# Kernel optimization log

Measured on AMD Instinct MI355X. Metric: run time of the kernel, lower is better.

The kernel has to match this reference:

```python
import jax, jax.numpy as jnp
import numpy as np

COMMITMENT_COST = 0.25
ENTROPY_LOSS_WEIGHT = 0.1
EPSILON = 1e-05
NUM_EMBEDDINGS = 2048
EMBEDDING_DIM = 64


def setup_inputs() -> dict:
    key = jax.random.key(0)
    kx, ke = jax.random.split(key)
    x = jax.random.normal(kx, (16, 64, 64, EMBEDDING_DIM), dtype=jnp.float32)
    embedding = jax.random.normal(ke, (NUM_EMBEDDINGS, EMBEDDING_DIM), dtype=jnp.float32)
    return {"x": x, "embedding": embedding}


def reference(x, embedding):
    input_shape = x.shape
    flat_x = x.reshape(-1, EMBEDDING_DIM)              # [N, D]
    distances = (jnp.sum(flat_x ** 2, axis=1, keepdims=True)
                 + jnp.sum(embedding ** 2, axis=1)
                 - 2.0 * jnp.matmul(flat_x, embedding.T))
    encoding_indices = jnp.argmin(distances, axis=1)   # [N]
    quantized = embedding[encoding_indices].reshape(input_shape)

    commitment_loss = jnp.mean((jax.lax.stop_gradient(quantized) - x) ** 2)
    codebook_loss = jnp.mean((quantized - jax.lax.stop_gradient(x)) ** 2)
    # straight-through estimator
    quantized = x + jax.lax.stop_gradient(quantized - x)

    # histogram of code usage == mean of one-hot encodings (scatter-add, avoids [N,K] one-hot)
    n_tokens = flat_x.shape[0]
    counts = jnp.zeros((NUM_EMBEDDINGS,), dtype=flat_x.dtype).at[encoding_indices].add(1.0)
    avg_probs = counts / n_tokens
    perplexity = jnp.exp(-jnp.sum(avg_probs * jnp.log(avg_probs + EPSILON)))
    entropy_loss = jnp.sum(avg_probs * jnp.log(avg_probs + EPSILON))

    vq_loss = codebook_loss + COMMITMENT_COST * commitment_loss + ENTROPY_LOSS_WEIGHT * entropy_loss
    return (quantized, vq_loss, commitment_loss, codebook_loss, perplexity,
            entropy_loss, encoding_indices.reshape(input_shape[:-1]), avg_probs)
```

## Files before the change

kernel.cpp:

```cpp
#include <hip/hip_runtime.h>
#include <float.h>

typedef _Float16 half8 __attribute__((ext_vector_type(8)));
typedef float    f32x4 __attribute__((ext_vector_type(4)));

constexpr int N_TOK = 65536;
constexpr int D     = 64;
constexpr int K     = 2048;
constexpr int TILE_C = 64;
constexpr int NTILE  = K / TILE_C;
constexpr int TOK_PER_BLK = 64;
constexpr int NBLK = N_TOK / TOK_PER_BLK;
constexpr float EPS_RESCORE = 0.15f;

constexpr size_t QN       = (size_t)N_TOK * D;
constexpr size_t SCAL_OFF = QN;
constexpr size_t IDX_OFF  = QN + 5;
constexpr size_t PROB_OFF = IDX_OFF + N_TOK;

constexpr size_t WS_HNORM = 0;
constexpr size_t WS_COUNT = 8192;
constexpr size_t WS_BSUM  = 16384;
constexpr size_t WS_SW    = 24576;
constexpr int REC_B  = 40;
constexpr int TILE_B = 256 * REC_B;

__device__ inline unsigned long long pack_key(float d, int k) {
    unsigned u = __float_as_uint(d);
    u = (u & 0x80000000u) ? ~u : (u | 0x80000000u);
    return ((unsigned long long)u << 32) | (unsigned)k;
}

__device__ inline float unpack_dist(unsigned long long key) {
    unsigned u = (unsigned)(key >> 32);
    u = (u & 0x80000000u) ? (u & 0x7FFFFFFFu) : ~u;
    return __uint_as_float(u);
}

__device__ inline unsigned long long shfl_xor_u64_w16(unsigned long long v, int m) {
    int lo = __shfl_xor((int)(unsigned)v, m, 16);
    int hi = __shfl_xor((int)(unsigned)(v >> 32), m, 16);
    return ((unsigned long long)(unsigned)hi << 32) | (unsigned)lo;
}

__global__ __launch_bounds__(256) void vq_init(const float* __restrict__ emb,
                                               float* __restrict__ hnorm,
                                               unsigned* __restrict__ counts,
                                               double* __restrict__ blocksums,
                                               char* __restrict__ swb) {
    const int g  = blockIdx.x * 256 + threadIdx.x;
    const int r  = g >> 3;
    const int c0 = g & 7;
    const float4* p4 = (const float4*)(emb + (size_t)r * D + 8 * c0);
    float4 q0 = p4[0], q1 = p4[1];
    float v[8] = {q0.x, q0.y, q0.z, q0.w, q1.x, q1.y, q1.z, q1.w};
    half8 h;
    float s = 0.f;
#pragma unroll
    for (int i = 0; i < 8; ++i) {
        s += v[i] * v[i];
        h[i] = (_Float16)v[i];
    }
    const int t    = r >> 6;
    const int w    = (r >> 4) & 3;
    const int m16  = r & 15;
    const int lane = (c0 & 3) * 16 + m16;
    const int slot = c0 >> 2;
    char* rec = swb + (size_t)(t * 256 + w * 64 + lane) * REC_B;
    *(half8*)(rec + slot * 16) = h;

#pragma unroll
    for (int off = 1; off < 8; off <<= 1) s += __shfl_xor(s, off, 8);
    if (c0 < 4) *(float*)(rec + 32) = 0.5f * s;
    if (c0 == 0) hnorm[r] = 0.5f * s;
    if (g < K) counts[g] = 0u;
    if (g < NBLK) blocksums[g] = 0.0;
}

#define ISSUE(P0, P1, HN)                                                          \
  {                                                                                \
    asm volatile("global_load_dwordx4 %0, %3, off\n\t"                             \
                 "global_load_dwordx4 %1, %3, off offset:16\n\t"                   \
                 "global_load_dword   %2, %3, off offset:32"                       \
                 : "=&v"(P0), "=&v"(P1), "=&v"(HN)                                 \
                 : "v"(pl));                                                       \
    pl += TILE_B;                                                                  \
  }

#define WAITC(N)                                                                   \
  asm volatile("s_waitcnt vmcnt(" #N ")" ::: "memory");                            \
  __builtin_amdgcn_sched_barrier(0);

#define VQ_STEP(P0, P1, HN, TT)                                                    \
  {                                                                                \
    f32x4 acc[4];                                                                  \
    __builtin_amdgcn_s_setprio(1);                                                 \
    _Pragma("unroll")                                                              \
    for (int a = 0; a < 4; ++a) {                                                  \
      acc[a] = (f32x4){(HN), (HN), (HN), (HN)};                                    \
      acc[a] = __builtin_amdgcn_mfma_f32_16x16x32_f16(axh[a][0], P0, acc[a], 0, 0, 0); \
      acc[a] = __builtin_amdgcn_mfma_f32_16x16x32_f16(axh[a][1], P1, acc[a], 0, 0, 0); \
    }                                                                              \
    __builtin_amdgcn_s_setprio(0);                                                 \
    _Pragma("unroll")                                                              \
    for (int a = 0; a < 4; ++a)                                                    \
      _Pragma("unroll")                                                            \
      for (int r = 0; r < 4; ++r) {                                                \
        unsigned _kb = (__float_as_uint(acc[a][r]) & 0xFFFFFFE0u) | (unsigned)(TT);\
        float _f = __uint_as_float(_kb);                                           \
        best2[a][r] = fminf(best2[a][r], fmaxf(best1[a][r], _f));                  \
        best1[a][r] = fminf(best1[a][r], _f);                                      \
      }                                                                            \
  }

__global__ __launch_bounds__(256, 2) void vq_fused(const float* __restrict__ x,
                                                   const float* __restrict__ emb,
                                                   const float* __restrict__ hnorm,
                                                   const char* __restrict__ swb,
                                                   unsigned* __restrict__ counts,
                                                   double* __restrict__ blocksums,
                                                   float* __restrict__ out) {
    __shared__ unsigned long long kls[64][10];
    __shared__ int bks[64];
    __shared__ double wsum[4];

    const int tid  = threadIdx.x;
    const int lane = tid & 63;
    const int wav  = tid >> 6;
    const int t0   = blockIdx.x * TOK_PER_BLK;
    const int m16  = lane & 15;
    const int g    = lane >> 4;
    const int ko   = g * 8;
    const int cit  = wav * 16 + m16;

    half8 axh[4][2];
#pragma unroll
    for (int a = 0; a < 4; ++a) {
        const float* xr = x + (size_t)(t0 + 16 * a + m16) * D;
#pragma unroll
        for (int c = 0; c < 2; ++c) {
            const float4* p4 = (const float4*)(xr + 32 * c + ko);
            float4 q0 = p4[0], q1 = p4[1];
            float v[8] = {q0.x, q0.y, q0.z, q0.w, q1.x, q1.y, q1.z, q1.w};
            half8 h;
#pragma unroll
            for (int j = 0; j < 8; ++j) h[j] = (_Float16)(-v[j]);
            axh[a][c] = h;
        }
    }

    float best1[4][4], best2[4][4];
#pragma unroll
    for (int a = 0; a < 4; ++a)
#pragma unroll
        for (int r = 0; r < 4; ++r) { best1[a][r] = FLT_MAX; best2[a][r] = FLT_MAX; }

    const char* pl = swb + (size_t)tid * REC_B;

    half8 A0, A1;  float hA;
    half8 B0, B1;  float hB;
    half8 C0, C1;  float hC;

    ISSUE(A0, A1, hA);
    ISSUE(B0, B1, hB);

    for (int t = 0; t < 28; t += 3) {
        ISSUE(C0, C1, hC);
        WAITC(6);
        VQ_STEP(A0, A1, hA, t);
        ISSUE(A0, A1, hA);
        WAITC(6);
        VQ_STEP(B0, B1, hB, t + 1);
        ISSUE(B0, B1, hB);
        WAITC(6);
        VQ_STEP(C0, C1, hC, t + 2);
    }
    WAITC(3);
    VQ_STEP(A0, A1, hA, 30);
    WAITC(0);
    VQ_STEP(B0, B1, hB, 31);

#pragma unroll
    for (int a = 0; a < 4; ++a)
#pragma unroll
        for (int r = 0; r < 4; ++r) {
            const unsigned b1 = __float_as_uint(best1[a][r]);
            const unsigned b2 = __float_as_uint(best2[a][r]);
            unsigned long long k1 = pack_key(best1[a][r], (int)(b1 & 31u) * TILE_C + cit);
            unsigned long long k2 = pack_key(best2[a][r], (int)(b2 & 31u) * TILE_C + cit);
#pragma unroll
            for (int off = 8; off; off >>= 1) {
                unsigned long long o1 = shfl_xor_u64_w16(k1, off);
                unsigned long long o2 = shfl_xor_u64_w16(k2, off);
                unsigned long long hi1 = (k1 > o1) ? k1 : o1;
                unsigned long long lo2 = (k2 < o2) ? k2 : o2;
                k1 = (k1 < o1) ? k1 : o1;
                k2 = (hi1 < lo2) ? hi1 : lo2;
            }
            if (m16 == 0) {
                kls[16 * a + g * 4 + r][wav]     = k1;
                kls[16 * a + g * 4 + r][4 + wav] = k2;
            }
        }
    __syncthreads();

    if (tid < 64) {
        float ds[8]; int kk[8];
        unsigned long long kmin = ~0ULL;
#pragma unroll
        for (int w = 0; w < 8; ++w) {
            unsigned long long key = kls[tid][w];
            ds[w] = unpack_dist(key);
            kk[w] = (int)(unsigned)(key & 0xFFFFFFFFu);
            if (key < kmin) kmin = key;
        }
        int bk = (int)(unsigned)(kmin & 0xFFFFFFFFu);
        const float fmin = unpack_dist(kmin);
        int cnt = 0;
#pragma unroll
        for (int w = 0; w < 8; ++w) cnt += (ds[w] <= fmin + EPS_RESCORE) ? 1 : 0;

        if (cnt > 1) {
            unsigned long long bkey = ~0ULL;
            const float* xr = x + (size_t)(t0 + tid) * D;
            for (int w = 0; w < 8; ++w) {
                if (ds[w] <= fmin + EPS_RESCORE) {
                    const int k = kk[w];
                    const float* cr = emb + (size_t)k * D;
                    float s0 = 0.f, s1 = 0.f, s2 = 0.f, s3 = 0.f;
#pragma unroll
                    for (int i = 0; i < 16; ++i) {
                        s0 = fmaf(cr[4 * i + 0], xr[4 * i + 0], s0);
                        s1 = fmaf(cr[4 * i + 1], xr[4 * i + 1], s1);
                        s2 = fmaf(cr[4 * i + 2], xr[4 * i + 2], s2);
                        s3 = fmaf(cr[4 * i + 3], xr[4 * i + 3], s3);
                    }
                    float hd = hnorm[k] - ((s0 + s1) + (s2 + s3));
                    unsigned long long key = pack_key(hd, k);
                    if (key < bkey) bkey = key;
                }
            }
            bk = (int)(unsigned)(bkey & 0xFFFFFFFFu);
        }
        bks[tid] = bk;
        out[IDX_OFF + t0 + tid] = (float)bk;
        atomicAdd(&counts[bk], 1u);
    }
    __syncthreads();

    const int tok = tid >> 2;
    const int i4  = tid & 3;
    const int bk  = bks[tok];
    const float4* xr4 = (const float4*)(x + (size_t)(t0 + tok) * D);
    const float4* cr4 = (const float4*)(emb + (size_t)bk * D);
    float4* qr4 = (float4*)(out + (size_t)(t0 + tok) * D);
    float local = 0.f;
#pragma unroll
    for (int ii = 0; ii < 4; ++ii) {
        const int idx = i4 + 4 * ii;
        float4 xv = xr4[idx];
        float4 cv = cr4[idx];
        float dx = cv.x - xv.x, dy = cv.y - xv.y;
        float dz = cv.z - xv.z, dw = cv.w - xv.w;
        local += dx * dx + dy * dy + dz * dz + dw * dw;
        float4 q;
        q.x = xv.x + dx; q.y = xv.y + dy;
        q.z = xv.z + dz; q.w = xv.w + dw;
        qr4[idx] = q;
    }
    double ld = (double)local;
#pragma unroll
    for (int off = 32; off > 0; off >>= 1) ld += __shfl_down(ld, off, 64);
    if (lane == 0) wsum[wav] = ld;
    __syncthreads();
    if (tid == 0)
        blocksums[blockIdx.x] = (wsum[0] + wsum[1]) + (wsum[2] + wsum[3]);
}

__global__ __launch_bounds__(256) void vq_finalize(const unsigned* __restrict__ counts,
                                                   const double* __restrict__ blocksums,
                                                   float* __restrict__ out) {
    const int tid = threadIdx.x;
    double e = 0.0;
#pragma unroll
    for (int i = 0; i < 8; ++i) {
        int k = tid + i * 256;
        float p = (float)counts[k] / 65536.0f;
        out[PROB_OFF + k] = p;
        double pd = (double)p;
        e += pd * log(pd + 1e-5);
    }
    double s = 0.0;
#pragma unroll
    for (int i = 0; i < NBLK / 256; ++i) s += blocksums[tid + i * 256];
#pragma unroll
    for (int off = 32; off > 0; off >>= 1) {
        e += __shfl_down(e, off, 64);
        s += __shfl_down(s, off, 64);
    }
    __shared__ double we[4], ws2[4];
    int lane = tid & 63, wid = tid >> 6;
    if (lane == 0) { we[wid] = e; ws2[wid] = s; }
    __syncthreads();
    if (tid == 0) {
        double entropy = (we[0] + we[1]) + (we[2] + we[3]);
        double sumsq   = (ws2[0] + ws2[1]) + (ws2[2] + ws2[3]);
        double mse     = sumsq / (double)((size_t)N_TOK * D);
        out[SCAL_OFF + 0] = (float)(1.25 * mse + 0.1 * entropy);
        out[SCAL_OFF + 1] = (float)mse;
        out[SCAL_OFF + 2] = (float)mse;
        out[SCAL_OFF + 3] = (float)exp(-entropy);
        out[SCAL_OFF + 4] = (float)entropy;
    }
}

extern "C" void kernel_launch(void* const* d_in, const int* in_sizes, int n_in,
                              void* d_out, int out_size, void* d_ws, size_t ws_size,
                              hipStream_t stream) {
    const float* x   = (const float*)d_in[0];
    const float* emb = (const float*)d_in[1];
    float* out = (float*)d_out;

    char* ws = (char*)d_ws;
    float*    hnorm     = (float*)(ws + WS_HNORM);
    unsigned* counts    = (unsigned*)(ws + WS_COUNT);
    double*   blocksums = (double*)(ws + WS_BSUM);
    char*     swb       = ws + WS_SW;

    vq_init<<<K * 8 / 256, 256, 0, stream>>>(emb, hnorm, counts, blocksums, swb);
    vq_fused<<<NBLK, 256, 0, stream>>>(x, emb, hnorm, swb, counts, blocksums, out);
    vq_finalize<<<1, 256, 0, stream>>>(counts, blocksums, out);
}
```

Measured before the change: 130.6 us.

## Deepen codebook prefetch to four stages and use SGPR-based global loads

```diff
diff --git a/kernel.cpp b/kernel.cpp
--- a/kernel.cpp
+++ b/kernel.cpp
@@ -77,15 +77,12 @@
     if (g < NBLK) blocksums[g] = 0.0;
 }
 
-#define ISSUE(P0, P1, HN)                                                          \
-  {                                                                                \
-    asm volatile("global_load_dwordx4 %0, %3, off\n\t"                             \
-                 "global_load_dwordx4 %1, %3, off offset:16\n\t"                   \
-                 "global_load_dword   %2, %3, off offset:32"                       \
-                 : "=&v"(P0), "=&v"(P1), "=&v"(HN)                                 \
-                 : "v"(pl));                                                       \
-    pl += TILE_B;                                                                  \
-  }
+#define ISSUE(P0, P1, HN, SB)                                                      \
+  asm volatile("global_load_dwordx4 %0, %3, %4\n\t"                                \
+               "global_load_dwordx4 %1, %3, %4 offset:16\n\t"                      \
+               "global_load_dword   %2, %3, %4 offset:32"                          \
+               : "=&v"(P0), "=&v"(P1), "=&v"(HN)                                   \
+               : "v"(voff), "s"(SB));
 
 #define WAITC(N)                                                                   \
   asm volatile("s_waitcnt vmcnt(" #N ")" ::: "memory");                            \
@@ -94,21 +91,19 @@
 #define VQ_STEP(P0, P1, HN, TT)                                                    \
   {                                                                                \
     f32x4 acc[4];                                                                  \
-    __builtin_amdgcn_s_setprio(1);                                                 \
     _Pragma("unroll")                                                              \
     for (int a = 0; a < 4; ++a) {                                                  \
       acc[a] = (f32x4){(HN), (HN), (HN), (HN)};                                    \
       acc[a] = __builtin_amdgcn_mfma_f32_16x16x32_f16(axh[a][0], P0, acc[a], 0, 0, 0); \
       acc[a] = __builtin_amdgcn_mfma_f32_16x16x32_f16(axh[a][1], P1, acc[a], 0, 0, 0); \
     }                                                                              \
-    __builtin_amdgcn_s_setprio(0);                                                 \
     _Pragma("unroll")                                                              \
     for (int a = 0; a < 4; ++a)                                                    \
       _Pragma("unroll")                                                            \
       for (int r = 0; r < 4; ++r) {                                                \
         unsigned _kb = (__float_as_uint(acc[a][r]) & 0xFFFFFFE0u) | (unsigned)(TT);\
         float _f = __uint_as_float(_kb);                                           \
-        best2[a][r] = fminf(best2[a][r], fmaxf(best1[a][r], _f));                  \
+        best2[a][r] = __builtin_amdgcn_fmed3f(best1[a][r], best2[a][r], _f);       \
         best1[a][r] = fminf(best1[a][r], _f);                                      \
       }                                                                            \
   }
@@ -155,30 +150,41 @@
 #pragma unroll
         for (int r = 0; r < 4; ++r) { best1[a][r] = FLT_MAX; best2[a][r] = FLT_MAX; }
 
-    const char* pl = swb + (size_t)tid * REC_B;
+    const unsigned voff = (unsigned)(tid * REC_B);
+    unsigned long long sb = (unsigned long long)swb;
 
     half8 A0, A1;  float hA;
     half8 B0, B1;  float hB;
     half8 C0, C1;  float hC;
-
-    ISSUE(A0, A1, hA);
-    ISSUE(B0, B1, hB);
-
-    for (int t = 0; t < 28; t += 3) {
-        ISSUE(C0, C1, hC);
-        WAITC(6);
+    half8 D0, D1;  float hD;
+
+    ISSUE(A0, A1, hA, sb); sb += TILE_B;
+    ISSUE(B0, B1, hB, sb); sb += TILE_B;
+    ISSUE(C0, C1, hC, sb); sb += TILE_B;
+
+    for (int t = 0; t < 28; t += 4) {
+        ISSUE(D0, D1, hD, sb); sb += TILE_B;
+        WAITC(9);
         VQ_STEP(A0, A1, hA, t);
-        ISSUE(A0, A1, hA);
-        WAITC(6);
+        ISSUE(A0, A1, hA, sb); sb += TILE_B;
+        WAITC(9);
         VQ_STEP(B0, B1, hB, t + 1);
-        ISSUE(B0, B1, hB);
-        WAITC(6);
+        ISSUE(B0, B1, hB, sb); sb += TILE_B;
+        WAITC(9);
         VQ_STEP(C0, C1, hC, t + 2);
-    }
+        ISSUE(C0, C1, hC, sb); sb += TILE_B;
+        WAITC(9);
+        VQ_STEP(D0, D1, hD, t + 3);
+    }
+    ISSUE(D0, D1, hD, sb);
+    WAITC(9);
+    VQ_STEP(A0, A1, hA, 28);
+    WAITC(6);
+    VQ_STEP(B0, B1, hB, 29);
     WAITC(3);
-    VQ_STEP(A0, A1, hA, 30);
+    VQ_STEP(C0, C1, hC, 30);
     WAITC(0);
-    VQ_STEP(B0, B1, hB, 31);
+    VQ_STEP(D0, D1, hD, 31);
 
 #pragma unroll
     for (int a = 0; a < 4; ++a)
```

Result: no change. 129.0 us (-1.2%).
